# Performance work log

Measured on AMD Instinct MI355X. Metric: run time of the kernel, lower is better.

Reference implementation:

```python
import jax, jax.numpy as jnp
import numpy as np

N = 50000
F_IN = 256
F_OUT = 256
K = 5
E = 1_600_000
SQRT_2PI = float(np.sqrt(2.0 * np.pi))
SQRT_2 = float(np.sqrt(2.0))


def _ex_relu(mu, sigma):
    # expected value of relu(Normal(mu, sigma)) with sigma = variance
    is_zero = sigma == 0
    safe_sigma = jnp.where(is_zero, 1e-10, sigma)
    sqrt_sigma = jnp.sqrt(safe_sigma)
    w = mu / sqrt_sigma
    nr = sqrt_sigma * (jnp.exp(-0.5 * w * w) / SQRT_2PI
                       + 0.5 * w * (1.0 + jax.lax.erf(w / SQRT_2)))
    return jnp.where(is_zero, jnp.maximum(mu, 0.0), nr)


def _conv(h, src, dst):
    # SimpleConv(aggr='add', combine_root='self_loop'):
    # out[d] = h[d] + sum_{(s,d) in edges} h[s];  h: [K, N, O]
    agg = jnp.zeros_like(h).at[:, dst, :].add(h[:, src, :])
    return h + agg


def setup_inputs() -> dict:
    key = jax.random.key(0)
    ks = jax.random.split(key, 7)
    x = jax.random.normal(ks[0], (N, F_IN), dtype=jnp.float32)
    edges = jax.random.randint(ks[1], (2, E), 0, N, dtype=jnp.int64)
    mask = jax.random.randint(ks[2], (N, F_IN), 0, 2) == 1  # True = missing
    logp = jax.random.normal(ks[3], (K,), dtype=jnp.float32)
    means = jax.random.normal(ks[4], (K, F_IN), dtype=jnp.float32)
    logvars = jax.random.normal(ks[5], (K, F_IN), dtype=jnp.float32)
    weight = jax.random.normal(ks[6], (F_IN, F_OUT), dtype=jnp.float32) * (1.414 / np.sqrt(F_IN + F_OUT) * np.sqrt(6.0))
    bias = jnp.zeros((F_OUT,), dtype=jnp.float32)
    return {"x": x, "edges": edges, "mask": mask, "logp": logp,
            "means": means, "logvars": logvars, "weight": weight, "bias": bias}


def reference(x, edges, mask, logp, means, logvars, weight, bias):
    src, dst = edges[0], edges[1]
    variances = jnp.exp(logvars)                                   # [K, F]
    m = mask[None, :, :]                                           # [1, N, F]
    mean_mat = jnp.where(m, means[:, None, :], x[None, :, :])      # [K, N, F]
    var_mat = jnp.where(m, variances[:, None, :], 0.0)             # [K, N, F]

    transform_x = jnp.einsum('knf,fo->kno', mean_mat, weight) + bias
    transform_covs = jnp.einsum('knf,fo->kno', var_mat, weight * weight)

    conv_x = _conv(transform_x, src, dst)                          # [K, N, O]
    conv_covs = _conv(transform_covs, src, dst)                    # [K, N, O]

    expected_x = _ex_relu(conv_x, conv_covs)                       # [K, N, O]

    # GMM responsibilities over components
    diff2 = (mean_mat - means[:, None, :]) ** 2 / variances[:, None, :]
    log_n = (-0.5 * jnp.sum(diff2, axis=2)
             - 0.5 * F_IN * np.log(2.0 * np.pi)
             - 0.5 * jnp.sum(logvars))                             # [K, N]
    gamma = jax.nn.softmax(logp[:, None] + log_n, axis=0)          # [K, N]

    return jnp.sum(expected_x * gamma[:, :, None], axis=0)         # [N, O]
```

## Files before the change

### kernel.cpp

```cpp
#include <hip/hip_runtime.h>
#include <math.h>

#define F 256
#define KMIX 5
#define RECB 640
#define GR 16
#define GS 3136

typedef __attribute__((ext_vector_type(8))) short bf16x8;
typedef __attribute__((ext_vector_type(4))) float f32x4;

__device__ __forceinline__ float bf2f(unsigned short u) {
  union { unsigned int i; float f; } v; v.i = ((unsigned int)u) << 16; return v.f;
}
__device__ __forceinline__ unsigned short f2bf(float f) {
  union { float f; unsigned int i; } v; v.f = f;
  unsigned int u = v.i;
  unsigned int r = (u + 0x7fffu + ((u >> 16) & 1u)) >> 16;
  return (unsigned short)r;
}

__device__ __forceinline__ f32x4 MFMA(bf16x8 a, bf16x8 b, f32x4 c) {
  return __builtin_amdgcn_mfma_f32_16x16x32_bf16(a, b, c, 0, 0, 0);
}

__device__ __forceinline__ float ex_relu_fast(float mu, float sig) {
  const float c1 = 1.2732395447f;
  const float c2 = 2.5464790895f;
  float t = mu * mu;
  float u = t + c1 * sig;
  float v = t + c2 * sig + 1e-20f;
  float r = __builtin_amdgcn_rsqf(v);
  return 0.5f * mu + 0.5f * u * r;
}

__global__ void kzero(unsigned int* p, long long n) {
  long long i = (long long)blockIdx.x * blockDim.x + threadIdx.x;
  long long stride = (long long)gridDim.x * blockDim.x;
  for (; i < n; i += stride) p[i] = 0u;
}

__global__ __launch_bounds__(256) void k_tab(const float* __restrict__ logvars,
                                             float* __restrict__ ivar) {
  int i = blockIdx.x * 256 + threadIdx.x;
  if (i < KMIX * F) ivar[i] = __expf(-logvars[i]);
}

__global__ __launch_bounds__(256) void k_prep(
    const float* __restrict__ x, const int* __restrict__ mask,
    const float* __restrict__ logp, const float* __restrict__ means,
    const float* __restrict__ ivar,
    unsigned char* __restrict__ rec, float* __restrict__ gamma, int Npad) {
  int n = blockIdx.x;
  int f = threadIdx.x;
  int idx = n * F + f;
  float xv = x[idx];
  int m = mask[idx];
  unsigned char* rn = rec + (size_t)n * RECB;
  ((unsigned short*)rn)[f] = m ? (unsigned short)0 : f2bf(xv);
  int wave = threadIdx.x >> 6;
  int lane = threadIdx.x & 63;
  unsigned long long bal = __ballot(m != 0);
  if (lane == 0) *(unsigned long long*)(rn + 512 + wave * 8) = bal;
  float cb[KMIX];
#pragma unroll
  for (int k = 0; k < KMIX; ++k) {
    float d = xv - means[k * F + f];
    cb[k] = m ? 0.0f : d * d * ivar[k * F + f];
  }
  __shared__ float red[KMIX][4];
#pragma unroll
  for (int k = 0; k < KMIX; ++k) {
    float c = cb[k];
    for (int off = 32; off > 0; off >>= 1) c += __shfl_down(c, off, 64);
    if (lane == 0) red[k][wave] = c;
  }
  __syncthreads();
  if (threadIdx.x == 0) {
    float lg[KMIX], mx = -1e30f;
#pragma unroll
    for (int k = 0; k < KMIX; ++k) {
      float tot = red[k][0] + red[k][1] + red[k][2] + red[k][3];
      lg[k] = logp[k] - 0.5f * tot;
      mx = fmaxf(mx, lg[k]);
    }
    float den = 0.0f, e[KMIX];
#pragma unroll
    for (int k = 0; k < KMIX; ++k) { e[k] = __expf(lg[k] - mx); den += e[k]; }
    float inv = 1.0f / den;
#pragma unroll
    for (int k = 0; k < KMIX; ++k) gamma[k * Npad + n] = e[k] * inv;
  }
}

__global__ void k_count(const int* __restrict__ edges, int* __restrict__ cnt, int E) {
  int i = blockIdx.x * blockDim.x + threadIdx.x;
  if (i < E) {
    int dst = edges[E + i];
    int g = edges[i] / GS;
    atomicAdd(&cnt[dst * GR + g], 1);
  }
}

__global__ __launch_bounds__(1024) void k_scanA(const int* __restrict__ cnt,
                                                int* __restrict__ excl,
                                                int* __restrict__ bsum, int n) {
  __shared__ int s[1024];
  int t = threadIdx.x;
  int i = blockIdx.x * 1024 + t;
  int v = (i < n) ? cnt[i] : 0;
  s[t] = v;
  __syncthreads();
  for (int off = 1; off < 1024; off <<= 1) {
    int u = (t >= off) ? s[t - off] : 0;
    __syncthreads();
    s[t] += u;
    __syncthreads();
  }
  if (i < n) excl[i] = s[t] - v;
  if (t == 1023) bsum[blockIdx.x] = s[1023];
}

__global__ __launch_bounds__(1024) void k_scanB(int* __restrict__ bsum, int nb) {
  __shared__ int s[1024];
  int t = threadIdx.x;
  int v = (t < nb) ? bsum[t] : 0;
  s[t] = v;
  __syncthreads();
  for (int off = 1; off < 1024; off <<= 1) {
    int u = (t >= off) ? s[t - off] : 0;
    __syncthreads();
    s[t] += u;
    __syncthreads();
  }
  if (t < nb) bsum[t] = s[t] - v;
}

__global__ __launch_bounds__(1024) void k_scanC(int* __restrict__ offs,
                                                int* __restrict__ cur,
                                                const int* __restrict__ bsum,
                                                int n, int E) {
  int i = blockIdx.x * 1024 + threadIdx.x;
  if (i < n) {
    int v = offs[i] + bsum[blockIdx.x];
    offs[i] = v;
    cur[i] = v;
  }
  if (i == 0) offs[n] = E;
}

__global__ void k_fill(const int* __restrict__ edges, int* __restrict__ cur,
                       int* __restrict__ srclist, int E) {
  int i = blockIdx.x * blockDim.x + threadIdx.x;
  if (i < E) {
    int src = edges[i];
    int dst = edges[E + i];
    int g = src / GS;
    int pos = atomicAdd(&cur[dst * GR + g], 1);
    srclist[pos] = src;
  }
}

__global__ __launch_bounds__(1024) void k_gather(
    const unsigned char* __restrict__ rec,
    const int* __restrict__ offs, const int* __restrict__ srclist,
    unsigned short* __restrict__ xs_pack, unsigned short* __restrict__ sm_pack,
    float* __restrict__ degp1) {
  __shared__ float xs_l[16][257];
  __shared__ float sm_l[16][257];
  int tile = blockIdx.x;
  int wave = threadIdx.x >> 6, lane = threadIdx.x & 63;
  int fb = lane * 4;
  int n = tile * 16 + wave;
  const unsigned char* rn = rec + (size_t)n * RECB;
  ushort4 xv = *(const ushort4*)(rn + lane * 8);
  unsigned int mw = *(const unsigned int*)(rn + 512 + ((lane >> 3) << 2));
  unsigned int nib = (mw >> ((lane & 7) * 4)) & 0xFu;
  unsigned int macc = (nib | (nib << 7) | (nib << 14) | (nib << 21)) & 0x01010101u;
  float a0 = bf2f(xv.x), a1 = bf2f(xv.y), a2 = bf2f(xv.z), a3 = bf2f(xv.w);
  int s0 = offs[n * GR], s1 = offs[n * GR + GR];
  int i = s0;
  for (; i + 4 <= s1; i += 4) {
    int sa = srclist[i], sb = srclist[i + 1], sc = srclist[i + 2], sd = srclist[i + 3];
    const unsigned char* ra = rec + (size_t)sa * RECB;
    const unsigned char* rb = rec + (size_t)sb * RECB;
    const unsigned char* rc = rec + (size_t)sc * RECB;
    const unsigned char* rd = rec + (size_t)sd * RECB;
    ushort4 va = *(const ushort4*)(ra + lane * 8);
    ushort4 vb = *(const ushort4*)(rb + lane * 8);
    ushort4 vc = *(const ushort4*)(rc + lane * 8);
    ushort4 vd = *(const ushort4*)(rd + lane * 8);
    unsigned int wa = *(const unsigned int*)(ra + 512 + ((lane >> 3) << 2));
    unsigned int wb = *(const unsigned int*)(rb + 512 + ((lane >> 3) << 2));
    unsigned int wc = *(const unsigned int*)(rc + 512 + ((lane >> 3) << 2));
    unsigned int wd = *(const unsigned int*)(rd + 512 + ((lane >> 3) << 2));
    a0 += bf2f(va.x) + bf2f(vb.x) + bf2f(vc.x) + bf2f(vd.x);
    a1 += bf2f(va.y) + bf2f(vb.y) + bf2f(vc.y) + bf2f(vd.y);
    a2 += bf2f(va.z) + bf2f(vb.z) + bf2f(vc.z) + bf2f(vd.z);
    a3 += bf2f(va.w) + bf2f(vb.w) + bf2f(vc.w) + bf2f(vd.w);
    unsigned int na = (wa >> ((lane & 7) * 4)) & 0xFu;
    unsigned int nb = (wb >> ((lane & 7) * 4)) & 0xFu;
    unsigned int nc = (wc >> ((lane & 7) * 4)) & 0xFu;
    unsigned int nd = (wd >> ((lane & 7) * 4)) & 0xFu;
    macc += (na | (na << 7) | (na << 14) | (na << 21)) & 0x01010101u;
    macc += (nb | (nb << 7) | (nb << 14) | (nb << 21)) & 0x01010101u;
    macc += (nc | (nc << 7) | (nc << 14) | (nc << 21)) & 0x01010101u;
    macc += (nd | (nd << 7) | (nd << 14) | (nd << 21)) & 0x01010101u;
  }
  for (; i < s1; ++i) {
    int s = srclist[i];
    const unsigned char* rs = rec + (size_t)s * RECB;
    ushort4 sv = *(const ushort4*)(rs + lane * 8);
    unsigned int ws = *(const unsigned int*)(rs + 512 + ((lane >> 3) << 2));
    a0 += bf2f(sv.x); a1 += bf2f(sv.y); a2 += bf2f(sv.z); a3 += bf2f(sv.w);
    unsigned int ns = (ws >> ((lane & 7) * 4)) & 0xFu;
    macc += (ns | (ns << 7) | (ns << 14) | (ns << 21)) & 0x01010101u;
  }
  xs_l[wave][fb] = a0; xs_l[wave][fb + 1] = a1; xs_l[wave][fb + 2] = a2; xs_l[wave][fb + 3] = a3;
  sm_l[wave][fb] = (float)(macc & 0xFFu);
  sm_l[wave][fb + 1] = (float)((macc >> 8) & 0xFFu);
  sm_l[wave][fb + 2] = (float)((macc >> 16) & 0xFFu);
  sm_l[wave][fb + 3] = (float)(macc >> 24);
  if (lane == 0) degp1[n] = (float)(s1 - s0 + 1);
  __syncthreads();
  if (threadIdx.x < 512) {
    int slot = threadIdx.x;
    int kt = slot >> 6, l = slot & 63;
    int r = l & 15, q = l >> 4;
    int fbase = kt * 32 + q * 8;
    bf16x8 vx, vs;
#pragma unroll
    for (int j = 0; j < 8; ++j) {
      vx[j] = (short)f2bf(xs_l[r][fbase + j]);
      vs[j] = (short)f2bf(sm_l[r][fbase + j]);
    }
    long long po = ((long long)tile * 8 + kt) * 64 + l;
    ((bf16x8*)xs_pack)[po] = vx;
    ((bf16x8*)sm_pack)[po] = vs;
  }
}

__global__ __launch_bounds__(64) void k_bpack(
    const float* __restrict__ weight, const float* __restrict__ means,
    const float* __restrict__ logvars, unsigned short* __restrict__ bpack) {
  int bid = blockIdx.x;
  int kt = bid & 7, ot = (bid >> 3) & 15, m = bid >> 7;
  int l = threadIdx.x;
  int r = l & 15, q = l >> 4;
  int o = ot * 16 + r;
  bf16x8 v;
#pragma unroll
  for (int j = 0; j < 8; ++j) {
    int f = kt * 32 + q * 8 + j;
    float wv = weight[f * F + o];
    float val;
    if (m == 0) val = wv;
    else if (m <= 5) val = means[(m - 1) * F + f] * wv;
    else val = __expf(logvars[(m - 6) * F + f]) * wv * wv;
    v[j] = (short)f2bf(val);
  }
  ((bf16x8*)bpack)[((long long)(m * 16 + ot) * 8 + kt) * 64 + l] = v;
}

__global__ __launch_bounds__(256, 2) void k_gemm(
    const unsigned short* __restrict__ xs_pack, const unsigned short* __restrict__ sm_pack,
    const unsigned short* __restrict__ bpack, const float* __restrict__ degp1,
    const float* __restrict__ gamma, const float* __restrict__ bias,
    float* __restrict__ out, int N, int Npad, int RB) {
  int L = blockIdx.x;
  int rb = (L >> 4) * 8 + (L & 7);
  int co = (L >> 3) & 1;
  if (rb >= RB) return;
  __shared__ unsigned char sp_lds[32768];
  int tid = threadIdx.x;
  int wave = tid >> 6, lane = tid & 63;
  int wr = wave >> 1, wc = wave & 1;
  int bo = co * 2 + wc;
  int q = lane >> 4, r16 = lane & 15;
  int rt0 = rb * 4 + wr * 2;
  const bf16x8* XP = (const bf16x8*)xs_pack;
  const bf16x8* BP = (const bf16x8*)bpack;

  {
    const uint4* src = (const uint4*)((const unsigned char*)sm_pack + (size_t)rb * 32768) + tid;
    uint4* dst = (uint4*)(void*)sp_lds + tid;
#pragma unroll
    for (int it = 0; it < 8; ++it) dst[it * 256] = src[it * 256];
  }

  f32x4 C1[2][4];
#pragma unroll
  for (int rt = 0; rt < 2; ++rt)
#pragma unroll
    for (int c = 0; c < 4; ++c) C1[rt][c] = (f32x4){0.f, 0.f, 0.f, 0.f};
#pragma unroll
  for (int kt = 0; kt < 8; ++kt) {
    bf16x8 a0 = XP[((size_t)rt0 * 8 + kt) * 64 + lane];
    bf16x8 a1 = XP[((size_t)(rt0 + 1) * 8 + kt) * 64 + lane];
#pragma unroll
    for (int c = 0; c < 4; ++c) {
      bf16x8 b = BP[((size_t)(bo * 4 + c) * 8 + kt) * 64 + lane];
      C1[0][c] = MFMA(a0, b, C1[0][c]);
      C1[1][c] = MFMA(a1, b, C1[1][c]);
    }
  }

  int row0 = rb * 64 + wr * 32 + q * 4;
  float dp[2][4];
#pragma unroll
  for (int rt = 0; rt < 2; ++rt)
#pragma unroll
    for (int rr = 0; rr < 4; ++rr) dp[rt][rr] = degp1[row0 + rt * 16 + rr];
  float bs[4];
#pragma unroll
  for (int c = 0; c < 4; ++c) bs[c] = bias[bo * 64 + c * 16 + r16];

  f32x4 outa[2][4];
#pragma unroll
  for (int rt = 0; rt < 2; ++rt)
#pragma unroll
    for (int c = 0; c < 4; ++c) outa[rt][c] = (f32x4){0.f, 0.f, 0.f, 0.f};

  __syncthreads();
  const unsigned char* myl = sp_lds + wr * 16384;

  for (int k = 0; k < KMIX; ++k) {
    float gm[2][4];
#pragma unroll
    for (int rt = 0; rt < 2; ++rt)
#pragma unroll
      for (int rr = 0; rr < 4; ++rr) gm[rt][rr] = gamma[k * Npad + row0 + rt * 16 + rr];
#pragma unroll
    for (int cp = 0; cp < 2; ++cp) {
      f32x4 ax[2][2], ac[2][2];
#pragma unroll
      for (int rt = 0; rt < 2; ++rt)
#pragma unroll
        for (int cc = 0; cc < 2; ++cc) {
          ax[rt][cc] = C1[rt][cp * 2 + cc];
          ac[rt][cc] = (f32x4){0.f, 0.f, 0.f, 0.f};
        }
#pragma unroll
      for (int kt = 0; kt < 8; ++kt) {
        bf16x8 sp0 = *(const bf16x8*)(myl + kt * 1024 + lane * 16);
        bf16x8 sp1 = *(const bf16x8*)(myl + 8192 + kt * 1024 + lane * 16);
#pragma unroll
        for (int cc = 0; cc < 2; ++cc) {
          int c = cp * 2 + cc;
          bf16x8 bw = BP[(((size_t)(1 + k) * 16 + (bo * 4 + c)) * 8 + kt) * 64 + lane];
          bf16x8 bv = BP[(((size_t)(6 + k) * 16 + (bo * 4 + c)) * 8 + kt) * 64 + lane];
          ax[0][cc] = MFMA(sp0, bw, ax[0][cc]);
          ax[1][cc] = MFMA(sp1, bw, ax[1][cc]);
          ac[0][cc] = MFMA(sp0, bv, ac[0][cc]);
          ac[1][cc] = MFMA(sp1, bv, ac[1][cc]);
        }
      }
#pragma unroll
      for (int rt = 0; rt < 2; ++rt)
#pragma unroll
        for (int cc = 0; cc < 2; ++cc)
#pragma unroll
          for (int rr = 0; rr < 4; ++rr) {
            int c = cp * 2 + cc;
            float mu = ax[rt][cc][rr] + dp[rt][rr] * bs[c];
            float e = ex_relu_fast(mu, ac[rt][cc][rr]);
            outa[rt][c][rr] += gm[rt][rr] * e;
          }
    }
  }

  int col = bo * 64 + r16;
#pragma unroll
  for (int rt = 0; rt < 2; ++rt)
#pragma unroll
    for (int c = 0; c < 4; ++c)
#pragma unroll
      for (int rr = 0; rr < 4; ++rr) {
        int row = row0 + rt * 16 + rr;
        if (row < N) out[(long long)row * F + col + c * 16] = outa[rt][c][rr];
      }
}

extern "C" void kernel_launch(void* const* d_in, const int* in_sizes, int n_in,
                              void* d_out, int out_size, void* d_ws, size_t ws_size,
                              hipStream_t stream) {
  const float* x = (const float*)d_in[0];
  const int* edges = (const int*)d_in[1];
  const int* mask = (const int*)d_in[2];
  const float* logp = (const float*)d_in[3];
  const float* means = (const float*)d_in[4];
  const float* logvars = (const float*)d_in[5];
  const float* weight = (const float*)d_in[6];
  const float* bias = (const float*)d_in[7];
  float* out = (float*)d_out;

  int N = in_sizes[0] / F;
  int E = in_sizes[1] / 2;
  int Npad = ((N + 127) / 128) * 128;
  int RB = Npad / 64;
  int NB = N * GR;
  int SB = (NB + 1023) / 1024;

  char* w = (char*)d_ws;
  auto alloc = [&](size_t bytes) {
    char* p = w;
    w += (bytes + 255) & ~(size_t)255;
    return p;
  };
  unsigned char* rec = (unsigned char*)alloc((size_t)N * RECB);
  unsigned short* xsp = (unsigned short*)alloc((size_t)Npad * F * 2);
  unsigned short* smp = (unsigned short*)alloc((size_t)Npad * F * 2);
  unsigned short* bpk = (unsigned short*)alloc((size_t)11 * F * F * 2);
  int* cnt = (int*)alloc((size_t)NB * 4);
  int* offs = (int*)alloc((size_t)(NB + 1) * 4);
  int* cur = (int*)alloc((size_t)NB * 4);
  int* bsum = (int*)alloc((size_t)1024 * 4);
  int* srclist = (int*)alloc((size_t)E * 4);
  float* degp1 = (float*)alloc((size_t)Npad * 4);
  float* gamma = (float*)alloc((size_t)KMIX * Npad * 4);
  float* ivar = (float*)alloc((size_t)KMIX * F * 4);

  kzero<<<782, 256, 0, stream>>>((unsigned int*)cnt, NB);
  k_tab<<<(KMIX * F + 255) / 256, 256, 0, stream>>>(logvars, ivar);
  k_prep<<<N, 256, 0, stream>>>(x, mask, logp, means, ivar, rec, gamma, Npad);
  k_count<<<(E + 255) / 256, 256, 0, stream>>>(edges, cnt, E);
  k_scanA<<<SB, 1024, 0, stream>>>(cnt, offs, bsum, NB);
  k_scanB<<<1, 1024, 0, stream>>>(bsum, SB);
  k_scanC<<<SB, 1024, 0, stream>>>(offs, cur, bsum, NB, E);
  k_fill<<<(E + 255) / 256, 256, 0, stream>>>(edges, cur, srclist, E);
  k_gather<<<N / 16, 1024, 0, stream>>>(rec, offs, srclist, xsp, smp, degp1);
  k_bpack<<<11 * 16 * 8, 64, 0, stream>>>(weight, means, logvars, bpk);
  int NGG = (RB + 7) / 8;
  k_gemm<<<NGG * 16, 256, 0, stream>>>(xsp, smp, bpk, degp1, gamma, bias, out, N, Npad, RB);
}
```

Measured before the change: 848.6 us.

## Shrink per-wave GEMM tile to one row tile and raise occupancy

The fused GEMM kernel now gives each wave a 16-row by 32-column tile processed in two column passes, where before it was 32 rows by 64 columns. The grid is doubled, each block covers one 64-column output slice, and launch bounds go from 2 to 3 blocks per CU. Fewer accumulators per thread cut register pressure so more waves can hide latency. The cost is less reuse of B-operand loads across row tiles, and every block copies the full 32 KB LDS tile of sparse rows, so LDS fill traffic doubles.

```diff
diff --git a/kernel.cpp b/kernel.cpp
--- a/kernel.cpp
+++ b/kernel.cpp
@@ -262,22 +262,20 @@
   ((bf16x8*)bpack)[((long long)(m * 16 + ot) * 8 + kt) * 64 + l] = v;
 }
 
-__global__ __launch_bounds__(256, 2) void k_gemm(
+__global__ __launch_bounds__(256, 3) void k_gemm(
     const unsigned short* __restrict__ xs_pack, const unsigned short* __restrict__ sm_pack,
     const unsigned short* __restrict__ bpack, const float* __restrict__ degp1,
     const float* __restrict__ gamma, const float* __restrict__ bias,
     float* __restrict__ out, int N, int Npad, int RB) {
   int L = blockIdx.x;
-  int rb = (L >> 4) * 8 + (L & 7);
-  int co = (L >> 3) & 1;
+  int rb = (L >> 5) * 8 + (L & 7);
+  int bo = (L >> 3) & 3;
   if (rb >= RB) return;
   __shared__ unsigned char sp_lds[32768];
   int tid = threadIdx.x;
   int wave = tid >> 6, lane = tid & 63;
-  int wr = wave >> 1, wc = wave & 1;
-  int bo = co * 2 + wc;
   int q = lane >> 4, r16 = lane & 15;
-  int rt0 = rb * 4 + wr * 2;
+  int rt0 = rb * 4 + wave;
   const bf16x8* XP = (const bf16x8*)xs_pack;
   const bf16x8* BP = (const bf16x8*)bpack;
 
@@ -288,97 +286,78 @@
     for (int it = 0; it < 8; ++it) dst[it * 256] = src[it * 256];
   }
 
-  f32x4 C1[2][4];
-#pragma unroll
-  for (int rt = 0; rt < 2; ++rt)
-#pragma unroll
-    for (int c = 0; c < 4; ++c) C1[rt][c] = (f32x4){0.f, 0.f, 0.f, 0.f};
-#pragma unroll
-  for (int kt = 0; kt < 8; ++kt) {
-    bf16x8 a0 = XP[((size_t)rt0 * 8 + kt) * 64 + lane];
-    bf16x8 a1 = XP[((size_t)(rt0 + 1) * 8 + kt) * 64 + lane];
-#pragma unroll
-    for (int c = 0; c < 4; ++c) {
-      bf16x8 b = BP[((size_t)(bo * 4 + c) * 8 + kt) * 64 + lane];
-      C1[0][c] = MFMA(a0, b, C1[0][c]);
-      C1[1][c] = MFMA(a1, b, C1[1][c]);
+  int row0 = rb * 64 + wave * 16 + q * 4;
+  float dp[4];
+#pragma unroll
+  for (int rr = 0; rr < 4; ++rr) dp[rr] = degp1[row0 + rr];
+
+  __syncthreads();
+  const unsigned char* myl = sp_lds + wave * 8192;
+
+  for (int cp = 0; cp < 2; ++cp) {
+    f32x4 C1[2];
+#pragma unroll
+    for (int cc = 0; cc < 2; ++cc) C1[cc] = (f32x4){0.f, 0.f, 0.f, 0.f};
+#pragma unroll
+    for (int kt = 0; kt < 8; ++kt) {
+      bf16x8 a = XP[((size_t)rt0 * 8 + kt) * 64 + lane];
+#pragma unroll
+      for (int cc = 0; cc < 2; ++cc) {
+        bf16x8 b = BP[((size_t)(bo * 4 + cp * 2 + cc) * 8 + kt) * 64 + lane];
+        C1[cc] = MFMA(a, b, C1[cc]);
+      }
     }
-  }
-
-  int row0 = rb * 64 + wr * 32 + q * 4;
-  float dp[2][4];
-#pragma unroll
-  for (int rt = 0; rt < 2; ++rt)
-#pragma unroll
-    for (int rr = 0; rr < 4; ++rr) dp[rt][rr] = degp1[row0 + rt * 16 + rr];
-  float bs[4];
-#pragma unroll
-  for (int c = 0; c < 4; ++c) bs[c] = bias[bo * 64 + c * 16 + r16];
-
-  f32x4 outa[2][4];
-#pragma unroll
-  for (int rt = 0; rt < 2; ++rt)
-#pragma unroll
-    for (int c = 0; c < 4; ++c) outa[rt][c] = (f32x4){0.f, 0.f, 0.f, 0.f};
-
-  __syncthreads();
-  const unsigned char* myl = sp_lds + wr * 16384;
-
-  for (int k = 0; k < KMIX; ++k) {
-    float gm[2][4];
-#pragma unroll
-    for (int rt = 0; rt < 2; ++rt)
-#pragma unroll
-      for (int rr = 0; rr < 4; ++rr) gm[rt][rr] = gamma[k * Npad + row0 + rt * 16 + rr];
-#pragma unroll
-    for (int cp = 0; cp < 2; ++cp) {
-      f32x4 ax[2][2], ac[2][2];
-#pragma unroll
-      for (int rt = 0; rt < 2; ++rt)
+
+    float bs[2];
+#pragma unroll
+    for (int cc = 0; cc < 2; ++cc) bs[cc] = bias[bo * 64 + cp * 32 + cc * 16 + r16];
+
+    f32x4 outa[2];
+#pragma unroll
+    for (int cc = 0; cc < 2; ++cc) outa[cc] = (f32x4){0.f, 0.f, 0.f, 0.f};
+
+    for (int k = 0; k < KMIX; ++k) {
+      float gm[4];
+#pragma unroll
+      for (int rr = 0; rr < 4; ++rr) gm[rr] = gamma[k * Npad + row0 + rr];
+      f32x4 ax[2], ac[2];
+#pragma unroll
+      for (int cc = 0; cc < 2; ++cc) {
+        ax[cc] = C1[cc];
+        ac[cc] = (f32x4){0.f, 0.f, 0.f, 0.f};
+      }
+#pragma unroll
+      for (int kt = 0; kt < 8; ++kt) {
+        bf16x8 sp = *(const bf16x8*)(myl + kt * 1024 + lane * 16);
 #pragma unroll
         for (int cc = 0; cc < 2; ++cc) {
-          ax[rt][cc] = C1[rt][cp * 2 + cc];
-          ac[rt][cc] = (f32x4){0.f, 0.f, 0.f, 0.f};
-        }
-#pragma unroll
-      for (int kt = 0; kt < 8; ++kt) {
-        bf16x8 sp0 = *(const bf16x8*)(myl + kt * 1024 + lane * 16);
-        bf16x8 sp1 = *(const bf16x8*)(myl + 8192 + kt * 1024 + lane * 16);
-#pragma unroll
-        for (int cc = 0; cc < 2; ++cc) {
-          int c = cp * 2 + cc;
-          bf16x8 bw = BP[(((size_t)(1 + k) * 16 + (bo * 4 + c)) * 8 + kt) * 64 + lane];
-          bf16x8 bv = BP[(((size_t)(6 + k) * 16 + (bo * 4 + c)) * 8 + kt) * 64 + lane];
-          ax[0][cc] = MFMA(sp0, bw, ax[0][cc]);
-          ax[1][cc] = MFMA(sp1, bw, ax[1][cc]);
-          ac[0][cc] = MFMA(sp0, bv, ac[0][cc]);
-          ac[1][cc] = MFMA(sp1, bv, ac[1][cc]);
+          int c = bo * 4 + cp * 2 + cc;
+          bf16x8 bw = BP[(((size_t)(1 + k) * 16 + c) * 8 + kt) * 64 + lane];
+          bf16x8 bv = BP[(((size_t)(6 + k) * 16 + c) * 8 + kt) * 64 + lane];
+          ax[cc] = MFMA(sp, bw, ax[cc]);
+          ac[cc] = MFMA(sp, bv, ac[cc]);
         }
       }
 #pragma unroll
-      for (int rt = 0; rt < 2; ++rt)
-#pragma unroll
-        for (int cc = 0; cc < 2; ++cc)
-#pragma unroll
-          for (int rr = 0; rr < 4; ++rr) {
-            int c = cp * 2 + cc;
-            float mu = ax[rt][cc][rr] + dp[rt][rr] * bs[c];
-            float e = ex_relu_fast(mu, ac[rt][cc][rr]);
-            outa[rt][c][rr] += gm[rt][rr] * e;
-          }
+      for (int cc = 0; cc < 2; ++cc)
+#pragma unroll
+        for (int rr = 0; rr < 4; ++rr) {
+          float mu = ax[cc][rr] + dp[rr] * bs[cc];
+          float e = ex_relu_fast(mu, ac[cc][rr]);
+          outa[cc][rr] += gm[rr] * e;
+        }
     }
-  }
-
-  int col = bo * 64 + r16;
-#pragma unroll
-  for (int rt = 0; rt < 2; ++rt)
-#pragma unroll
-    for (int c = 0; c < 4; ++c)
+
+#pragma unroll
+    for (int cc = 0; cc < 2; ++cc) {
+      int col = bo * 64 + cp * 32 + cc * 16 + r16;
 #pragma unroll
       for (int rr = 0; rr < 4; ++rr) {
-        int row = row0 + rt * 16 + rr;
-        if (row < N) out[(long long)row * F + col + c * 16] = outa[rt][c][rr];
+        int row = row0 + rr;
+        if (row < N) out[(long long)row * F + col] = outa[cc][rr];
       }
+    }
+  }
 }
 
 extern "C" void kernel_launch(void* const* d_in, const int* in_sizes, int n_in,
@@ -431,5 +410,5 @@
   k_gather<<<N / 16, 1024, 0, stream>>>(rec, offs, srclist, xsp, smp, degp1);
   k_bpack<<<11 * 16 * 8, 64, 0, stream>>>(weight, means, logvars, bpk);
   int NGG = (RB + 7) / 8;
-  k_gemm<<<NGG * 16, 256, 0, stream>>>(xsp, smp, bpk, degp1, gamma, bias, out, N, Npad, RB);
-}
+  k_gemm<<<NGG * 32, 256, 0, stream>>>(xsp, smp, bpk, degp1, gamma, bias, out, N, Npad, RB);
+}
```

New measurement: 806.8 us. -4.9%, faster.

## Split k_gemm column tiles per block to cut registers and raise occupancy

Applied to the files above, without the earlier changes.

Each GEMM block now covers 64 output columns instead of 128, with each wave handling 32 columns. The grid doubles, per-wave accumulator state halves, and the kernel asks for three blocks per CU instead of two. The aim is more occupancy and parallelism to hide memory and MFMA latency. In exchange, the 32 KB LDS staging of the sparse-aggregated tile and the x-tile loads are repeated by twice as many blocks.

```diff
diff --git a/kernel.cpp b/kernel.cpp
--- a/kernel.cpp
+++ b/kernel.cpp
@@ -262,22 +262,22 @@
   ((bf16x8*)bpack)[((long long)(m * 16 + ot) * 8 + kt) * 64 + l] = v;
 }
 
-__global__ __launch_bounds__(256, 2) void k_gemm(
+__global__ __launch_bounds__(256, 3) void k_gemm(
     const unsigned short* __restrict__ xs_pack, const unsigned short* __restrict__ sm_pack,
     const unsigned short* __restrict__ bpack, const float* __restrict__ degp1,
     const float* __restrict__ gamma, const float* __restrict__ bias,
     float* __restrict__ out, int N, int Npad, int RB) {
   int L = blockIdx.x;
-  int rb = (L >> 4) * 8 + (L & 7);
-  int co = (L >> 3) & 1;
+  int rb = (L >> 5) * 8 + (L & 7);
+  int bo = (L >> 3) & 3;
   if (rb >= RB) return;
   __shared__ unsigned char sp_lds[32768];
   int tid = threadIdx.x;
   int wave = tid >> 6, lane = tid & 63;
-  int wr = wave >> 1, wc = wave & 1;
-  int bo = co * 2 + wc;
+  int rw = wave >> 1, cw = wave & 1;
   int q = lane >> 4, r16 = lane & 15;
-  int rt0 = rb * 4 + wr * 2;
+  int rt0 = rb * 4 + rw * 2;
+  int ct0 = bo * 4 + cw * 2;
   const bf16x8* XP = (const bf16x8*)xs_pack;
   const bf16x8* BP = (const bf16x8*)bpack;
 
@@ -288,41 +288,41 @@
     for (int it = 0; it < 8; ++it) dst[it * 256] = src[it * 256];
   }
 
-  f32x4 C1[2][4];
+  f32x4 C1[2][2];
 #pragma unroll
   for (int rt = 0; rt < 2; ++rt)
 #pragma unroll
-    for (int c = 0; c < 4; ++c) C1[rt][c] = (f32x4){0.f, 0.f, 0.f, 0.f};
+    for (int cc = 0; cc < 2; ++cc) C1[rt][cc] = (f32x4){0.f, 0.f, 0.f, 0.f};
 #pragma unroll
   for (int kt = 0; kt < 8; ++kt) {
     bf16x8 a0 = XP[((size_t)rt0 * 8 + kt) * 64 + lane];
     bf16x8 a1 = XP[((size_t)(rt0 + 1) * 8 + kt) * 64 + lane];
 #pragma unroll
-    for (int c = 0; c < 4; ++c) {
-      bf16x8 b = BP[((size_t)(bo * 4 + c) * 8 + kt) * 64 + lane];
-      C1[0][c] = MFMA(a0, b, C1[0][c]);
-      C1[1][c] = MFMA(a1, b, C1[1][c]);
+    for (int cc = 0; cc < 2; ++cc) {
+      bf16x8 b = BP[((size_t)(ct0 + cc) * 8 + kt) * 64 + lane];
+      C1[0][cc] = MFMA(a0, b, C1[0][cc]);
+      C1[1][cc] = MFMA(a1, b, C1[1][cc]);
     }
   }
 
-  int row0 = rb * 64 + wr * 32 + q * 4;
+  int row0 = rb * 64 + rw * 32 + q * 4;
   float dp[2][4];
 #pragma unroll
   for (int rt = 0; rt < 2; ++rt)
 #pragma unroll
     for (int rr = 0; rr < 4; ++rr) dp[rt][rr] = degp1[row0 + rt * 16 + rr];
-  float bs[4];
-#pragma unroll
-  for (int c = 0; c < 4; ++c) bs[c] = bias[bo * 64 + c * 16 + r16];
-
-  f32x4 outa[2][4];
+  float bs[2];
+#pragma unroll
+  for (int cc = 0; cc < 2; ++cc) bs[cc] = bias[bo * 64 + cw * 32 + cc * 16 + r16];
+
+  f32x4 outa[2][2];
 #pragma unroll
   for (int rt = 0; rt < 2; ++rt)
 #pragma unroll
-    for (int c = 0; c < 4; ++c) outa[rt][c] = (f32x4){0.f, 0.f, 0.f, 0.f};
+    for (int cc = 0; cc < 2; ++cc) outa[rt][cc] = (f32x4){0.f, 0.f, 0.f, 0.f};
 
   __syncthreads();
-  const unsigned char* myl = sp_lds + wr * 16384;
+  const unsigned char* myl = sp_lds + rw * 16384;
 
   for (int k = 0; k < KMIX; ++k) {
     float gm[2][4];
@@ -330,55 +330,52 @@
     for (int rt = 0; rt < 2; ++rt)
 #pragma unroll
       for (int rr = 0; rr < 4; ++rr) gm[rt][rr] = gamma[k * Npad + row0 + rt * 16 + rr];
-#pragma unroll
-    for (int cp = 0; cp < 2; ++cp) {
-      f32x4 ax[2][2], ac[2][2];
-#pragma unroll
-      for (int rt = 0; rt < 2; ++rt)
-#pragma unroll
-        for (int cc = 0; cc < 2; ++cc) {
-          ax[rt][cc] = C1[rt][cp * 2 + cc];
-          ac[rt][cc] = (f32x4){0.f, 0.f, 0.f, 0.f};
+    f32x4 ax[2][2], ac[2][2];
+#pragma unroll
+    for (int rt = 0; rt < 2; ++rt)
+#pragma unroll
+      for (int cc = 0; cc < 2; ++cc) {
+        ax[rt][cc] = C1[rt][cc];
+        ac[rt][cc] = (f32x4){0.f, 0.f, 0.f, 0.f};
+      }
+#pragma unroll
+    for (int kt = 0; kt < 8; ++kt) {
+      bf16x8 sp0 = *(const bf16x8*)(myl + kt * 1024 + lane * 16);
+      bf16x8 sp1 = *(const bf16x8*)(myl + 8192 + kt * 1024 + lane * 16);
+#pragma unroll
+      for (int cc = 0; cc < 2; ++cc) {
+        int c = ct0 + cc;
+        bf16x8 bw = BP[(((size_t)(1 + k) * 16 + c) * 8 + kt) * 64 + lane];
+        bf16x8 bv = BP[(((size_t)(6 + k) * 16 + c) * 8 + kt) * 64 + lane];
+        ax[0][cc] = MFMA(sp0, bw, ax[0][cc]);
+        ax[1][cc] = MFMA(sp1, bw, ax[1][cc]);
+        ac[0][cc] = MFMA(sp0, bv, ac[0][cc]);
+        ac[1][cc] = MFMA(sp1, bv, ac[1][cc]);
+      }
+    }
+#pragma unroll
+    for (int rt = 0; rt < 2; ++rt)
+#pragma unroll
+      for (int cc = 0; cc < 2; ++cc)
+#pragma unroll
+        for (int rr = 0; rr < 4; ++rr) {
+          float mu = ax[rt][cc][rr] + dp[rt][rr] * bs[cc];
+          float e = ex_relu_fast(mu, ac[rt][cc][rr]);
+          outa[rt][cc][rr] += gm[rt][rr] * e;
         }
-#pragma unroll
-      for (int kt = 0; kt < 8; ++kt) {
-        bf16x8 sp0 = *(const bf16x8*)(myl + kt * 1024 + lane * 16);
-        bf16x8 sp1 = *(const bf16x8*)(myl + 8192 + kt * 1024 + lane * 16);
-#pragma unroll
-        for (int cc = 0; cc < 2; ++cc) {
-          int c = cp * 2 + cc;
-          bf16x8 bw = BP[(((size_t)(1 + k) * 16 + (bo * 4 + c)) * 8 + kt) * 64 + lane];
-          bf16x8 bv = BP[(((size_t)(6 + k) * 16 + (bo * 4 + c)) * 8 + kt) * 64 + lane];
-          ax[0][cc] = MFMA(sp0, bw, ax[0][cc]);
-          ax[1][cc] = MFMA(sp1, bw, ax[1][cc]);
-          ac[0][cc] = MFMA(sp0, bv, ac[0][cc]);
-          ac[1][cc] = MFMA(sp1, bv, ac[1][cc]);
-        }
-      }
-#pragma unroll
-      for (int rt = 0; rt < 2; ++rt)
-#pragma unroll
-        for (int cc = 0; cc < 2; ++cc)
-#pragma unroll
-          for (int rr = 0; rr < 4; ++rr) {
-            int c = cp * 2 + cc;
-            float mu = ax[rt][cc][rr] + dp[rt][rr] * bs[c];
-            float e = ex_relu_fast(mu, ac[rt][cc][rr]);
-            outa[rt][c][rr] += gm[rt][rr] * e;
-          }
-    }
-  }
-
-  int col = bo * 64 + r16;
+  }
+
 #pragma unroll
   for (int rt = 0; rt < 2; ++rt)
 #pragma unroll
-    for (int c = 0; c < 4; ++c)
+    for (int cc = 0; cc < 2; ++cc) {
+      int col = bo * 64 + cw * 32 + cc * 16 + r16;
 #pragma unroll
       for (int rr = 0; rr < 4; ++rr) {
         int row = row0 + rt * 16 + rr;
-        if (row < N) out[(long long)row * F + col + c * 16] = outa[rt][c][rr];
+        if (row < N) out[(long long)row * F + col] = outa[rt][cc][rr];
       }
+    }
 }
 
 extern "C" void kernel_launch(void* const* d_in, const int* in_sizes, int n_in,
@@ -431,5 +428,5 @@
   k_gather<<<N / 16, 1024, 0, stream>>>(rec, offs, srclist, xsp, smp, degp1);
   k_bpack<<<11 * 16 * 8, 64, 0, stream>>>(weight, means, logvars, bpk);
   int NGG = (RB + 7) / 8;
-  k_gemm<<<NGG * 16, 256, 0, stream>>>(xsp, smp, bpk, degp1, gamma, bias, out, N, Npad, RB);
-}
+  k_gemm<<<NGG * 32, 256, 0, stream>>>(xsp, smp, bpk, degp1, gamma, bias, out, N, Npad, RB);
+}
```

Result: faster. 774.1 us (-8.8%).
